# Optimization experiments

Measured on AMD Instinct MI355X. Metric: run time of the kernel, lower is better.

The kernel has to match this reference:

```python
import jax, jax.numpy as jnp
import numpy as np

EPS = 1e-4   # synsin-style z clamp in world_to_view
BIG = 1e10   # z-buffer init


def _xy_grid(h, w):
    xs = jnp.linspace(-1.0, 1.0, w)
    ys = jnp.linspace(-1.0, 1.0, h)
    gy, gx = jnp.meshgrid(ys, xs, indexing='ij')
    return jnp.stack([gx.ravel(), gy.ravel()], 0)  # [2, h*w], NDC pixel rays


def _view_to_world(depth, K_inv, RTinv, xy):
    # depth [B,1,N]; homogeneous coords rows = (x*d, y*d, d, 1)
    proj = jnp.concatenate([xy[None] * depth, depth, jnp.ones_like(depth)], axis=1)  # [B,4,N]
    cam = jnp.einsum('bij,bjn->bin', K_inv, proj)
    return jnp.einsum('bij,bjn->bin', RTinv, cam)  # [B,4,N]


def _world_to_view(world, K, RT):
    cam2 = jnp.einsum('bij,bjn->bin', RT, world)
    xy_proj = jnp.einsum('bij,bjn->bin', K, cam2)
    z = xy_proj[:, 2:3]
    mask = jnp.abs(z) < EPS
    zs = jnp.where(mask, EPS, z)
    sampler = jnp.concatenate([xy_proj[:, 0:2] / zs, z], axis=1)  # [B,3,N]
    return jnp.where(mask, -10.0, sampler)


def _splat_one(sampler, feats, h, w):
    # sampler [3,N] (x,y in NDC, z depth); feats [C,N]. Nearest-pixel z-buffer splat.
    x, y, z = sampler[0], sampler[1], sampler[2]
    n = x.shape[0]
    px = jnp.round((x + 1.0) * 0.5 * (w - 1)).astype(jnp.int32)
    py = jnp.round((y + 1.0) * 0.5 * (h - 1)).astype(jnp.int32)
    valid = (px >= 0) & (px < w) & (py >= 0) & (py < h) & (z > EPS)
    idx = jnp.where(valid, py * w + px, h * w)  # invalid -> dump bucket h*w
    zv = jnp.where(valid, z, BIG)
    zbuf = jnp.full(h * w + 1, BIG, feats.dtype).at[idx].min(zv)
    pid = jnp.where(valid & (zv <= zbuf[idx]), jnp.arange(n, dtype=jnp.int32), n)
    win = jnp.full(h * w + 1, n, jnp.int32).at[idx].min(pid)[: h * w]  # winning point per pixel
    fpad = jnp.concatenate([feats, jnp.zeros((feats.shape[0], 1), feats.dtype)], axis=1)
    out = fpad[:, win].reshape(feats.shape[0], h, w)
    zb = zbuf[: h * w]
    depth = jnp.where(zb < BIG, zb, 0.0).reshape(1, h, w)
    return out, depth


def _project(depths, colors, feats, K, src_RTs, src_RTinvs, dst_RTs, dst_RTinvs):
    B, V, _, Hc, Wc = depths.shape
    _, _, C, Hf, Wf = feats.shape
    sh, sw = Hf / Hc, Wf / Wc
    scale = jnp.array([sw, sh, 1.0, 1.0], depths.dtype)[None, :, None]
    sK = K * scale
    sKinv = jnp.linalg.inv(sK)

    colors_r = jax.image.resize(colors.reshape(B * V, 3, Hc, Wc), (B * V, 3, Hf, Wf),
                                method='linear', antialias=True)
    depths_r = jax.image.resize(depths.reshape(B * V, 1, Hc, Wc), (B * V, 1, Hf, Wf),
                                method='nearest')
    feats_f = feats.reshape(B, V, C, Hf * Wf)
    colors_f = colors_r.reshape(B, V, 3, Hf * Wf)
    depths_f = depths_r.reshape(B, V, 1, Hf * Wf)

    xy = _xy_grid(Hf, Wf)
    dstRT = dst_RTs[:, 0]  # num_outputs == 1
    splat = jax.vmap(lambda s, f: _splat_one(s, f, Hf, Wf))

    results, warped, pdepths = [], [], []
    for i in range(V):  # small fixed number of source views
        world = _view_to_world(depths_f[:, i], sKinv, src_RTinvs[:, i], xy)
        sampler = _world_to_view(world, sK, dstRT)            # [B,3,N]
        src = jnp.concatenate([feats_f[:, i], colors_f[:, i] * 0.5 + 0.5], axis=1)  # [B,C+3,N]
        res, dep = splat(sampler, src)                        # [B,C+3,Hf,Wf], [B,1,Hf,Wf]
        results.append(res[:, :C])
        warped.append(res[:, C:])
        pdepths.append(dep)

    prj_fs = jnp.stack(results, 0)      # [V,B,C,Hf,Wf]
    warped = jnp.stack(warped, 0)       # [V,B,3,Hf,Wf]
    prj_depths = jnp.stack(pdepths, 0)  # [V,B,1,Hf,Wf]
    # forward() permutes prj_fs / prj_depths to [B,V,...]; warped stays [V,B,...]
    return prj_fs.transpose(1, 0, 2, 3, 4), warped, prj_depths.transpose(1, 0, 2, 3, 4)


def setup_inputs() -> dict:
    key = jax.random.key(0)
    k1, k2, k3 = jax.random.split(key, 3)
    B, V, Hc, Wc = 2, 2, 512, 512
    Hf, Wf, C = 256, 256, 64

    depths = jax.random.uniform(k1, (B, V, 1, Hc, Wc), jnp.float32, 1.0, 5.0)
    colors = jax.random.uniform(k2, (B, V, 3, Hc, Wc), jnp.float32, -1.0, 1.0)
    feats = jax.random.normal(k3, (B, V, C, Hf, Wf), jnp.float32)

    K = np.eye(4, dtype=np.float32)  # NDC intrinsic (fx=fy=1, cx=cy=0)
    th = 0.1
    R = np.array([[np.cos(th), 0, np.sin(th), 0.2],
                  [0, 1, 0, 0.0],
                  [-np.sin(th), 0, np.cos(th), 0.1],
                  [0, 0, 0, 1]], dtype=np.float32)
    src_RT = np.eye(4, dtype=np.float32)

    Kb = jnp.asarray(np.tile(K[None], (B, 1, 1)))
    src_RTs = jnp.asarray(np.tile(src_RT[None, None], (B, V, 1, 1)))
    src_RTinvs = src_RTs  # identity
    dst_RTs = jnp.asarray(np.tile(R[None, None], (B, 1, 1, 1)))
    dst_RTinvs = jnp.asarray(np.tile(np.linalg.inv(R)[None, None], (B, 1, 1, 1)))

    return {"depths": depths, "colors": colors, "feats": feats, "K": Kb,
            "src_RTs": src_RTs, "src_RTinvs": src_RTinvs,
            "dst_RTs": dst_RTs, "dst_RTinvs": dst_RTinvs}


def reference(depths, colors, feats, K, src_RTs, src_RTinvs, dst_RTs, dst_RTinvs):
    return _project(depths, colors, feats, K, src_RTs, src_RTinvs, dst_RTs, dst_RTinvs)
```

## Files before the change

### kernel.cpp

```cpp
#include <hip/hip_runtime.h>
#include <stdint.h>

#pragma clang fp contract(off)

namespace {
constexpr int B_ = 2, V_ = 2, HC = 512, WC = 512, HF = 256, WF = 256, CF = 64;
constexpr int NPIX = HF * WF;
constexpr float EPSF = 1e-4f;
constexpr float BIGF = 1e10f;
constexpr int NPT = B_ * V_ * NPIX;
constexpr int NBLK_PT = NPT / 256;
}

__device__ __forceinline__ float dot4f(const float* __restrict__ r,
                                       float v0, float v1, float v2, float v3) {
  float t = r[0] * v0;
  t = t + r[1] * v1;
  t = t + r[2] * v2;
  t = t + r[3] * v3;
  return t;
}

__global__ void prep_k(const float* __restrict__ K,
                       const float* __restrict__ colors,
                       float* __restrict__ colr,
                       float* __restrict__ mats,
                       unsigned long long* __restrict__ zwin) {
  int g = blockIdx.x * blockDim.x + threadIdx.x;

  if (g < NPT) zwin[g] = ~0ULL;

  if (g < B_) {
    int b = g;
    const float rowscale[4] = {0.5f, 0.5f, 1.0f, 1.0f};
    float sK[16];
    for (int i = 0; i < 4; ++i)
      for (int j = 0; j < 4; ++j)
        sK[i*4+j] = K[b*16 + i*4 + j] * rowscale[i];
    double m[16];
    for (int i = 0; i < 16; ++i) m[i] = (double)sK[i];
    double inv[16];
    inv[0]  =  m[5]*m[10]*m[15] - m[5]*m[11]*m[14] - m[9]*m[6]*m[15] + m[9]*m[7]*m[14] + m[13]*m[6]*m[11] - m[13]*m[7]*m[10];
    inv[4]  = -m[4]*m[10]*m[15] + m[4]*m[11]*m[14] + m[8]*m[6]*m[15] - m[8]*m[7]*m[14] - m[12]*m[6]*m[11] + m[12]*m[7]*m[10];
    inv[8]  =  m[4]*m[9]*m[15]  - m[4]*m[11]*m[13] - m[8]*m[5]*m[15] + m[8]*m[7]*m[13] + m[12]*m[5]*m[11] - m[12]*m[7]*m[9];
    inv[12] = -m[4]*m[9]*m[14]  + m[4]*m[10]*m[13] + m[8]*m[5]*m[14] - m[8]*m[6]*m[13] - m[12]*m[5]*m[10] + m[12]*m[6]*m[9];
    inv[1]  = -m[1]*m[10]*m[15] + m[1]*m[11]*m[14] + m[9]*m[2]*m[15] - m[9]*m[3]*m[14] - m[13]*m[2]*m[11] + m[13]*m[3]*m[10];
    inv[5]  =  m[0]*m[10]*m[15] - m[0]*m[11]*m[14] - m[8]*m[2]*m[15] + m[8]*m[3]*m[14] + m[12]*m[2]*m[11] - m[12]*m[3]*m[10];
    inv[9]  = -m[0]*m[9]*m[15]  + m[0]*m[11]*m[13] + m[8]*m[1]*m[15] - m[8]*m[3]*m[13] - m[12]*m[1]*m[11] + m[12]*m[3]*m[9];
    inv[13] =  m[0]*m[9]*m[14]  - m[0]*m[10]*m[13] - m[8]*m[1]*m[14] + m[8]*m[2]*m[13] + m[12]*m[1]*m[10] - m[12]*m[2]*m[9];
    inv[2]  =  m[1]*m[6]*m[15]  - m[1]*m[7]*m[14]  - m[5]*m[2]*m[15] + m[5]*m[3]*m[14] + m[13]*m[2]*m[7]  - m[13]*m[3]*m[6];
    inv[6]  = -m[0]*m[6]*m[15]  + m[0]*m[7]*m[14]  + m[4]*m[2]*m[15] - m[4]*m[3]*m[14] - m[12]*m[2]*m[7]  + m[12]*m[3]*m[6];
    inv[10] =  m[0]*m[5]*m[15]  - m[0]*m[7]*m[13]  - m[4]*m[1]*m[15] + m[4]*m[3]*m[13] + m[12]*m[1]*m[7]  - m[12]*m[3]*m[5];
    inv[14] = -m[0]*m[5]*m[14]  + m[0]*m[6]*m[13]  + m[4]*m[1]*m[14] - m[4]*m[2]*m[13] - m[12]*m[1]*m[6]  + m[12]*m[2]*m[5];
    inv[3]  = -m[1]*m[6]*m[11]  + m[1]*m[7]*m[10]  + m[5]*m[2]*m[11] - m[5]*m[3]*m[10] - m[9]*m[2]*m[7]   + m[9]*m[3]*m[6];
    inv[7]  =  m[0]*m[6]*m[11]  - m[0]*m[7]*m[10]  - m[4]*m[2]*m[11] + m[4]*m[3]*m[10] + m[8]*m[2]*m[7]   - m[8]*m[3]*m[6];
    inv[11] = -m[0]*m[5]*m[11]  + m[0]*m[7]*m[9]   + m[4]*m[1]*m[11] - m[4]*m[3]*m[9]  - m[8]*m[1]*m[7]   + m[8]*m[3]*m[5];
    inv[15] =  m[0]*m[5]*m[10]  - m[0]*m[6]*m[9]   - m[4]*m[1]*m[10] + m[4]*m[2]*m[9]  + m[8]*m[1]*m[6]   - m[8]*m[2]*m[5];
    double det = m[0]*inv[0] + m[1]*inv[4] + m[2]*inv[8] + m[3]*inv[12];
    double idet = 1.0 / det;
    for (int i = 0; i < 16; ++i) {
      mats[b*32 + i]      = sK[i];
      mats[b*32 + 16 + i] = (float)(inv[i] * idet);
    }
  }

  if (g >= B_ * V_ * 3 * NPIX) return;
  int pc  = g >> 16;
  int pix = g & (NPIX - 1);
  int y = pix >> 8, x = pix & (WF - 1);
  const float* src = colors + (size_t)pc * HC * WC;
  const float W37 = (float)(3.0 / 7.0), W17 = (float)(1.0 / 7.0);
  float wy[4] = {0.125f, 0.375f, 0.375f, 0.125f};
  float wx[4] = {0.125f, 0.375f, 0.375f, 0.125f};
  if (y == 0)      { wy[0] = 0.f; wy[1] = W37; wy[2] = W37; wy[3] = W17; }
  if (y == HF - 1) { wy[0] = W17; wy[1] = W37; wy[2] = W37; wy[3] = 0.f; }
  if (x == 0)      { wx[0] = 0.f; wx[1] = W37; wx[2] = W37; wx[3] = W17; }
  if (x == WF - 1) { wx[0] = W17; wx[1] = W37; wx[2] = W37; wx[3] = 0.f; }
  int jy0 = 2 * y - 1, jx0 = 2 * x - 1;
  float acc = 0.f;
  #pragma unroll
  for (int ty = 0; ty < 4; ++ty) {
    if (wy[ty] == 0.f) continue;
    int jy = jy0 + ty;
    float rs = 0.f;
    #pragma unroll
    for (int tx = 0; tx < 4; ++tx) {
      if (wx[tx] == 0.f) continue;
      rs = rs + wx[tx] * src[(size_t)jy * WC + (jx0 + tx)];
    }
    acc = acc + wy[ty] * rs;
  }
  colr[g] = acc;
}

__global__ void splat_k(const float* __restrict__ depths,
                        const float* __restrict__ mats,
                        const float* __restrict__ srcRTinv,
                        const float* __restrict__ dstRT,
                        unsigned long long* __restrict__ zwin) {
  int g = blockIdx.x * blockDim.x + threadIdx.x;
  if (g >= NPT) return;
  int bv = g >> 16;
  int n  = g & (NPIX - 1);
  int b  = bv / V_;
  int y = n >> 8, x = n & (WF - 1);
  float d = depths[(size_t)bv * HC * WC + (size_t)(2 * y + 1) * WC + (2 * x + 1)];
  const float step32 = 2.0f / 255.0f;
  float xf = (float)x * step32 - 1.0f;
  float yf = (float)y * step32 - 1.0f;
  float pr0 = xf * d, pr1 = yf * d, pr2 = d, pr3 = 1.0f;
  const float* sK  = mats + b * 32;
  const float* sKi = mats + b * 32 + 16;
  const float* Rs  = srcRTinv + (size_t)bv * 16;
  const float* Rd  = dstRT + (size_t)b * 16;
  float a0 = dot4f(sKi + 0,  pr0, pr1, pr2, pr3);
  float a1 = dot4f(sKi + 4,  pr0, pr1, pr2, pr3);
  float a2 = dot4f(sKi + 8,  pr0, pr1, pr2, pr3);
  float a3 = dot4f(sKi + 12, pr0, pr1, pr2, pr3);
  float w0 = dot4f(Rs + 0,  a0, a1, a2, a3);
  float w1 = dot4f(Rs + 4,  a0, a1, a2, a3);
  float w2 = dot4f(Rs + 8,  a0, a1, a2, a3);
  float w3 = dot4f(Rs + 12, a0, a1, a2, a3);
  float c0 = dot4f(Rd + 0,  w0, w1, w2, w3);
  float c1 = dot4f(Rd + 4,  w0, w1, w2, w3);
  float c2 = dot4f(Rd + 8,  w0, w1, w2, w3);
  float c3 = dot4f(Rd + 12, w0, w1, w2, w3);
  float p0 = dot4f(sK + 0, c0, c1, c2, c3);
  float p1 = dot4f(sK + 4, c0, c1, c2, c3);
  float p2 = dot4f(sK + 8, c0, c1, c2, c3);
  if (!(p2 > EPSF)) return;
  float sx = p0 / p2, sy = p1 / p2;
  float pxf = rintf(((sx + 1.0f) * 0.5f) * 255.0f);
  float pyf = rintf(((sy + 1.0f) * 0.5f) * 255.0f);
  if (!(pxf >= 0.0f && pxf <= 255.0f && pyf >= 0.0f && pyf <= 255.0f)) return;
  int idx = (int)pyf * WF + (int)pxf;
  unsigned zbits = __float_as_uint(p2);
  unsigned long long key = ((unsigned long long)zbits << 32) | (unsigned)n;
  atomicMin(&zwin[(size_t)bv * NPIX + idx], key);
}

__global__ void gather_k(const unsigned long long* __restrict__ zwin,
                         const float* __restrict__ feats,
                         const float* __restrict__ colr,
                         float* __restrict__ out0,
                         float* __restrict__ out1,
                         float* __restrict__ out2) {
  int bid = blockIdx.x;
  int grp = bid >> 10;
  int g   = (bid & (NBLK_PT - 1)) * 256 + threadIdx.x;
  int bv  = g >> 16;
  int pix = g & (NPIX - 1);
  unsigned long long key = zwin[g];
  bool hit = (key != ~0ULL);
  int n = (int)(key & 0xffffffffULL);

  if (grp < 4) {
    int c0 = grp * 16;
    const float* fb = feats + (size_t)bv * CF * NPIX + (size_t)c0 * NPIX;
    float* o0 = out0 + (size_t)bv * CF * NPIX + (size_t)c0 * NPIX + pix;
    if (hit) {
      #pragma unroll
      for (int c = 0; c < 16; ++c)
        __builtin_nontemporal_store(fb[(size_t)c * NPIX + n], &o0[(size_t)c * NPIX]);
    } else {
      #pragma unroll
      for (int c = 0; c < 16; ++c)
        __builtin_nontemporal_store(0.0f, &o0[(size_t)c * NPIX]);
    }
  } else {
    int b = bv >> 1, v = bv & 1;
    const float* cb = colr + (size_t)bv * 3 * NPIX;
    float* o1 = out1 + (size_t)(v * B_ + b) * 3 * NPIX + pix;
    if (hit) {
      float z = __uint_as_float((unsigned)(key >> 32));
      __builtin_nontemporal_store((z < BIGF) ? z : 0.0f, &out2[g]);
      #pragma unroll
      for (int ch = 0; ch < 3; ++ch)
        __builtin_nontemporal_store(cb[(size_t)ch * NPIX + n] * 0.5f + 0.5f,
                                    &o1[(size_t)ch * NPIX]);
    } else {
      __builtin_nontemporal_store(0.0f, &out2[g]);
      #pragma unroll
      for (int ch = 0; ch < 3; ++ch)
        __builtin_nontemporal_store(0.0f, &o1[(size_t)ch * NPIX]);
    }
  }
}

extern "C" void kernel_launch(void* const* d_in, const int* in_sizes, int n_in,
                              void* d_out, int out_size, void* d_ws, size_t ws_size,
                              hipStream_t stream) {
  const float* depths     = (const float*)d_in[0];
  const float* colors     = (const float*)d_in[1];
  const float* feats      = (const float*)d_in[2];
  const float* K          = (const float*)d_in[3];
  const float* src_RTinvs = (const float*)d_in[5];
  const float* dst_RTs    = (const float*)d_in[6];

  float* out0 = (float*)d_out;
  float* out1 = out0 + (size_t)B_ * V_ * CF * NPIX;
  float* out2 = out1 + (size_t)V_ * B_ * 3 * NPIX;

  unsigned long long* zwin = (unsigned long long*)d_ws;
  float* colr = (float*)(zwin + NPT);
  float* mats = colr + (size_t)B_ * V_ * 3 * NPIX;

  prep_k<<<(B_ * V_ * 3 * NPIX) / 256, 256, 0, stream>>>(K, colors, colr, mats, zwin);
  splat_k<<<NBLK_PT, 256, 0, stream>>>(depths, mats, src_RTinvs, dst_RTs, zwin);
  gather_k<<<5 * NBLK_PT, 256, 0, stream>>>(zwin, feats, colr, out0, out1, out2);
}
```

Baseline: 209.3 us.

## Transpose features to point-major layout before gathering splatted pixels

Adds a kernel that transposes the feature tensor from channel-major to point-major through LDS, so the gather reads one contiguous 256-byte row per winning point instead of 64 strided scattered loads. The gather is fused into one launch per pixel that writes all channels, colors and depth with nontemporal stores. The cost is an extra full read and write of the 64-channel feature tensor plus the workspace space to hold it, and 64 floats of registers per thread. The new path runs only when the workspace is large enough, otherwise the old gather runs.

Result: faster. 184.7 us (-11.8%).

```diff
diff --git a/kernel.cpp b/kernel.cpp
--- a/kernel.cpp
+++ b/kernel.cpp
@@ -10,6 +10,8 @@
 constexpr float BIGF = 1e10f;
 constexpr int NPT = B_ * V_ * NPIX;
 constexpr int NBLK_PT = NPT / 256;
+constexpr size_t WS_BASE = (size_t)NPT * 8 + (size_t)B_ * V_ * 3 * NPIX * 4 + 256;
+constexpr size_t TF_BYTES = (size_t)NPT * CF * 4;
 }
 
 __device__ __forceinline__ float dot4f(const float* __restrict__ r,
@@ -91,6 +93,35 @@
     acc = acc + wy[ty] * rs;
   }
   colr[g] = acc;
+}
+
+__global__ void transp_k(const float* __restrict__ feats,
+                         float* __restrict__ tf) {
+  __shared__ float lds[CF][65];
+  int bid = blockIdx.x;
+  int bv = bid >> 10;
+  int pix0 = (bid & 1023) << 6;
+  int t = threadIdx.x;
+  int sub = t >> 4;
+  int l16 = t & 15;
+  const float* fb = feats + (size_t)bv * CF * NPIX;
+  #pragma unroll
+  for (int pass = 0; pass < 4; ++pass) {
+    int ch = pass * 16 + sub;
+    const float4 v = *(const float4*)(fb + (size_t)ch * NPIX + pix0 + 4 * l16);
+    lds[ch][4*l16+0] = v.x; lds[ch][4*l16+1] = v.y;
+    lds[ch][4*l16+2] = v.z; lds[ch][4*l16+3] = v.w;
+  }
+  __syncthreads();
+  float* tb = tf + ((size_t)bv * NPIX + pix0) * CF;
+  #pragma unroll
+  for (int pass = 0; pass < 4; ++pass) {
+    int p = pass * 16 + sub;
+    float4 w;
+    w.x = lds[4*l16+0][p]; w.y = lds[4*l16+1][p];
+    w.z = lds[4*l16+2][p]; w.w = lds[4*l16+3][p];
+    *(float4*)(tb + (size_t)p * CF + 4 * l16) = w;
+  }
 }
 
 __global__ void splat_k(const float* __restrict__ depths,
@@ -139,6 +170,51 @@
   atomicMin(&zwin[(size_t)bv * NPIX + idx], key);
 }
 
+__global__ void gatherT_k(const unsigned long long* __restrict__ zwin,
+                          const float* __restrict__ tf,
+                          const float* __restrict__ colr,
+                          float* __restrict__ out0,
+                          float* __restrict__ out1,
+                          float* __restrict__ out2) {
+  int g = blockIdx.x * 256 + threadIdx.x;
+  int bv = g >> 16;
+  int pix = g & (NPIX - 1);
+  unsigned long long key = zwin[g];
+  bool hit = (key != ~0ULL);
+  int n = (int)(key & 0xffffffffULL);
+  float4 f[16];
+  if (hit) {
+    const float4* src = (const float4*)(tf + ((size_t)bv * NPIX + n) * CF);
+    #pragma unroll
+    for (int i = 0; i < 16; ++i) f[i] = src[i];
+  } else {
+    #pragma unroll
+    for (int i = 0; i < 16; ++i) f[i] = make_float4(0.f, 0.f, 0.f, 0.f);
+  }
+  float* o0 = out0 + (size_t)bv * CF * NPIX + pix;
+  const float* fs = (const float*)f;
+  #pragma unroll
+  for (int c = 0; c < CF; ++c)
+    __builtin_nontemporal_store(fs[c], &o0[(size_t)c * NPIX]);
+
+  int b = bv >> 1, v = bv & 1;
+  const float* cb = colr + (size_t)bv * 3 * NPIX;
+  float* o1 = out1 + (size_t)(v * B_ + b) * 3 * NPIX + pix;
+  if (hit) {
+    float z = __uint_as_float((unsigned)(key >> 32));
+    __builtin_nontemporal_store((z < BIGF) ? z : 0.0f, &out2[g]);
+    #pragma unroll
+    for (int ch = 0; ch < 3; ++ch)
+      __builtin_nontemporal_store(cb[(size_t)ch * NPIX + n] * 0.5f + 0.5f,
+                                  &o1[(size_t)ch * NPIX]);
+  } else {
+    __builtin_nontemporal_store(0.0f, &out2[g]);
+    #pragma unroll
+    for (int ch = 0; ch < 3; ++ch)
+      __builtin_nontemporal_store(0.0f, &o1[(size_t)ch * NPIX]);
+  }
+}
+
 __global__ void gather_k(const unsigned long long* __restrict__ zwin,
                          const float* __restrict__ feats,
                          const float* __restrict__ colr,
@@ -204,8 +280,16 @@
   unsigned long long* zwin = (unsigned long long*)d_ws;
   float* colr = (float*)(zwin + NPT);
   float* mats = colr + (size_t)B_ * V_ * 3 * NPIX;
+  float* tf   = (float*)((char*)d_ws + WS_BASE);
+
+  const bool use_tf = (ws_size >= WS_BASE + TF_BYTES);
 
   prep_k<<<(B_ * V_ * 3 * NPIX) / 256, 256, 0, stream>>>(K, colors, colr, mats, zwin);
+  if (use_tf)
+    transp_k<<<B_ * V_ * (NPIX / 64), 256, 0, stream>>>(feats, tf);
   splat_k<<<NBLK_PT, 256, 0, stream>>>(depths, mats, src_RTinvs, dst_RTs, zwin);
-  gather_k<<<5 * NBLK_PT, 256, 0, stream>>>(zwin, feats, colr, out0, out1, out2);
-}
+  if (use_tf)
+    gatherT_k<<<NBLK_PT, 256, 0, stream>>>(zwin, tf, colr, out0, out1, out2);
+  else
+    gather_k<<<5 * NBLK_PT, 256, 0, stream>>>(zwin, feats, colr, out0, out1, out2);
+}
```
